# Kernel tuning notes

Hardware: AMD Instinct MI355X
Metric: run time of the kernel (lower is better)

## Reference

```python
import jax, jax.numpy as jnp
import numpy as np

D_EMBED = 768
N_HEAD = 12
D_ATTN = D_EMBED // N_HEAD  # 64
SCALE = 1.0 / np.sqrt(D_ATTN)


def setup_inputs() -> dict:
    key = jax.random.key(0)
    ks = jax.random.split(key, 5)
    B, S = 1, 4096
    x = jax.random.normal(ks[0], (B, S, D_EMBED), dtype=jnp.float32)
    # Linear weights stored as [in, out]; init std 0.02 as in _init_weights
    Wq = jax.random.normal(ks[1], (D_EMBED, D_EMBED), dtype=jnp.float32) * 0.02
    Wk = jax.random.normal(ks[2], (D_EMBED, D_EMBED), dtype=jnp.float32) * 0.02
    Wv = jax.random.normal(ks[3], (D_EMBED, D_EMBED), dtype=jnp.float32) * 0.02
    Wo = jax.random.normal(ks[4], (D_EMBED, D_EMBED), dtype=jnp.float32) * 0.02
    gamma = jnp.ones((N_HEAD,), dtype=jnp.float32)
    return {"x": x, "Wq": Wq, "Wk": Wk, "Wv": Wv, "Wo": Wo, "gamma": gamma}


def reference(x, Wq, Wk, Wv, Wo, gamma):
    B, S, _ = x.shape
    # QKV projections (self-attention: k = v = q = x)
    def split_heads(y):
        return y.reshape(B, S, N_HEAD, D_ATTN).transpose(0, 2, 1, 3)  # [B,H,S,D]
    q = split_heads(x @ Wq)
    k = split_heads(x @ Wk)
    v = split_heads(x @ Wv)
    # RBF attention scores: exp(-gamma * scale * ||q - k||^2)
    q_norm = jnp.sum(q * q, axis=-1, keepdims=True)            # [B,H,S,1]
    k_norm = jnp.sum(k * k, axis=-1, keepdims=True)            # [B,H,S,1]
    qk = jnp.einsum('bhsd,bhtd->bhst', q, k)                   # [B,H,S,S]
    dist = jnp.maximum(q_norm - 2.0 * qk + jnp.swapaxes(k_norm, -2, -1), 0.0)
    g = gamma.reshape(1, N_HEAD, 1, 1)
    scores = jnp.exp(-g * SCALE * dist)                        # [B,H,S,S]
    # attn @ V, merge heads, output proj (dropout p=0 -> identity)
    out = jnp.einsum('bhst,bhtd->bhsd', scores, v)
    out = out.transpose(0, 2, 1, 3).reshape(B, S, D_EMBED)
    return out @ Wo
```

## Files before the change

### kernel.cpp

```cpp
#include <hip/hip_runtime.h>
#include <stdint.h>


typedef __attribute__((ext_vector_type(4))) float f32x4;
typedef __attribute__((ext_vector_type(8))) short s16x8;
typedef __attribute__((ext_vector_type(2))) unsigned int u32x2;
typedef __attribute__((ext_vector_type(4))) unsigned int u32x4;

#define S_LEN 4096
#define NHEAD 12
#define DE 768

__device__ __forceinline__ uint16_t f2bf(float f) {
  unsigned u = __float_as_uint(f);
  u += 0x7fffu + ((u >> 16) & 1u);
  return (uint16_t)(u >> 16);
}

__device__ __forceinline__ unsigned cvt_pk_bf16(float a, float b) {
  unsigned r;
  asm("v_cvt_pk_bf16_f32 %0, %1, %2" : "=v"(r) : "v"(a), "v"(b));
  return r;
}

__device__ __forceinline__ void gll16(const void* g, void* l) {
  __builtin_amdgcn_global_load_lds(
      (const __attribute__((address_space(1))) unsigned int*)g,
      (__attribute__((address_space(3))) unsigned int*)l, 16, 0, 0);
}

__global__ void k_cvt_x(const float* __restrict__ x, uint16_t* __restrict__ xb) {
  int i = (blockIdx.x * 256 + threadIdx.x) * 4;
  float4 v = *(const float4*)(x + i);
  u32x2 o;
  o.x = (unsigned)f2bf(v.x) | ((unsigned)f2bf(v.y) << 16);
  o.y = (unsigned)f2bf(v.z) | ((unsigned)f2bf(v.w) << 16);
  *(u32x2*)(xb + i) = o;
}

__global__ void k_cvt_w(const float* __restrict__ W0, const float* __restrict__ W1,
                        const float* __restrict__ W2, const float* __restrict__ W3,
                        uint16_t* __restrict__ T0, uint16_t* __restrict__ T1,
                        uint16_t* __restrict__ T2, uint16_t* __restrict__ T3) {
  __shared__ float tile[64][65];
  int z = blockIdx.z;
  const float* W = z == 0 ? W0 : z == 1 ? W1 : z == 2 ? W2 : W3;
  uint16_t* T = z == 0 ? T0 : z == 1 ? T1 : z == 2 ? T2 : T3;
  int r0 = blockIdx.y * 64, c0 = blockIdx.x * 64;
  int t = threadIdx.x;
#pragma unroll
  for (int ii = 0; ii < 16; ++ii) {
    int idx = ii * 256 + t;
    int r = idx >> 6, c = idx & 63;
    tile[r][c] = W[(r0 + r) * DE + c0 + c];
  }
  __syncthreads();
#pragma unroll
  for (int ii = 0; ii < 16; ++ii) {
    int idx = ii * 256 + t;
    int r = idx >> 6, c = idx & 63;
    T[(size_t)(c0 + r) * DE + (r0 + c)] = f2bf(tile[c][r]);
  }
}

template <int MODE>
__global__ __launch_bounds__(256) void k_gemm(
    const uint16_t* __restrict__ A, const uint16_t* __restrict__ B0,
    const uint16_t* __restrict__ B1, const uint16_t* __restrict__ B2,
    uint16_t* __restrict__ Oq, uint16_t* __restrict__ Ok, uint16_t* __restrict__ Ov,
    float* __restrict__ OF) {
  __shared__ __align__(16) uint16_t As[128 * 64];
  __shared__ __align__(16) uint16_t Bs[128 * 64];
  const int K = DE;
  int z = (MODE == 0) ? blockIdx.z : 0;
  const uint16_t* Bt = (MODE == 0) ? (z == 0 ? B0 : z == 1 ? B1 : B2) : B0;
  int m0 = blockIdx.x * 128, n0 = blockIdx.y * 128;
  int tid = threadIdx.x, lane = tid & 63, wid = tid >> 6;
  int G = lane >> 4, c = lane & 15;
  int wr = (wid >> 1) * 64, wc = (wid & 1) * 64;
  f32x4 acc[4][4] = {};
  const char* AsB = (const char*)As;
  const char* BsB = (const char*)Bs;
  for (int kt = 0; kt < K / 64; ++kt) {
#pragma unroll
    for (int i = 0; i < 4; ++i) {
      int L = (i * 256 + tid) * 16;
      int row = L >> 7, ch = (L >> 4) & 7;
      int gch = ch ^ (row & 7);
      gll16((const char*)A + ((size_t)(m0 + row) * K + kt * 64) * 2 + gch * 16,
            (char*)As + i * 4096 + wid * 1024);
      gll16((const char*)Bt + ((size_t)(n0 + row) * K + kt * 64) * 2 + gch * 16,
            (char*)Bs + i * 4096 + wid * 1024);
    }
    __syncthreads();
#pragma unroll
    for (int ks = 0; ks < 2; ++ks) {
      s16x8 a[4], b[4];
#pragma unroll
      for (int mi = 0; mi < 4; ++mi) {
        int row = wr + mi * 16 + c;
        a[mi] = *(const s16x8*)(AsB + row * 128 + (((G + 4 * ks) ^ (row & 7)) << 4));
      }
#pragma unroll
      for (int ni = 0; ni < 4; ++ni) {
        int row = wc + ni * 16 + c;
        b[ni] = *(const s16x8*)(BsB + row * 128 + (((G + 4 * ks) ^ (row & 7)) << 4));
      }
#pragma unroll
      for (int mi = 0; mi < 4; ++mi)
#pragma unroll
        for (int ni = 0; ni < 4; ++ni)
          acc[mi][ni] = __builtin_amdgcn_mfma_f32_16x16x32_bf16(a[mi], b[ni], acc[mi][ni], 0, 0, 0);
    }
    __syncthreads();
  }
#pragma unroll
  for (int mi = 0; mi < 4; ++mi) {
#pragma unroll
    for (int ni = 0; ni < 4; ++ni) {
      int r = m0 + wr + mi * 16 + G * 4;
      int n = n0 + wc + ni * 16 + c;
      if (MODE == 0) {
        int h = n >> 6, d = n & 63;
        if (z < 2) {
          uint16_t* O = (z == 0) ? Oq : Ok;
#pragma unroll
          for (int rr = 0; rr < 4; ++rr)
            O[((size_t)h * S_LEN + (r + rr)) * 64 + d] = f2bf(acc[mi][ni][rr]);
        } else {
          u32x2 pk;
          pk.x = (unsigned)f2bf(acc[mi][ni][0]) | ((unsigned)f2bf(acc[mi][ni][1]) << 16);
          pk.y = (unsigned)f2bf(acc[mi][ni][2]) | ((unsigned)f2bf(acc[mi][ni][3]) << 16);
          *(u32x2*)(Ov + ((size_t)(h * 64 + d)) * S_LEN + r) = pk;
        }
      } else {
#pragma unroll
        for (int rr = 0; rr < 4; ++rr) OF[(size_t)(r + rr) * DE + n] = acc[mi][ni][rr];
      }
    }
  }
}

__global__ void k_norm(const uint16_t* __restrict__ q, const uint16_t* __restrict__ k,
                       const float* __restrict__ gamma,
                       float* __restrict__ cqn, float* __restrict__ ckn) {
  int row = blockIdx.x * 256 + threadIdx.x;
  const int total = NHEAD * S_LEN;
  const uint16_t* src = (row < total) ? q : k;
  float* dst = (row < total) ? cqn : ckn;
  int r = (row < total) ? row : row - total;
  float coef = -gamma[r >> 12] * 0.18033688011112043f;
  const u32x4* p = (const u32x4*)(src + (size_t)r * 64);
  float s = 0.f;
#pragma unroll
  for (int i = 0; i < 8; ++i) {
    u32x4 v = p[i];
#pragma unroll
    for (int j = 0; j < 4; ++j) {
      unsigned w = v[j];
      float a = __uint_as_float(w << 16);
      float b = __uint_as_float(w & 0xffff0000u);
      s += a * a + b * b;
    }
  }
  dst[r] = coef * s;
}

__global__ __launch_bounds__(256, 3) void k_attn(
    const uint16_t* __restrict__ q, const uint16_t* __restrict__ k,
    const uint16_t* __restrict__ vT, const float* __restrict__ cqn,
    const float* __restrict__ ckn, const float* __restrict__ gamma,
    uint16_t* __restrict__ att) {
  __shared__ __align__(16) uint16_t Ks[128 * 64];
  __shared__ __align__(16) uint16_t Vs[64 * 128];
  __shared__ __align__(16) uint16_t Ps[4][32 * 64];
  __shared__ __align__(16) float cks[128];
  int h = blockIdx.y;
  int tid = threadIdx.x, lane = tid & 63, wid = tid >> 6;
  int G = lane >> 4, c = lane & 15;
  int wq = wid & 1, wkv = wid >> 1;
  int qg0 = blockIdx.x * 64 + wq * 32 + c;

  s16x8 qf[2][2];
  const char* qb0 = (const char*)(q + ((size_t)h * S_LEN + qg0) * 64);
#pragma unroll
  for (int ks = 0; ks < 2; ++ks) {
    qf[0][ks] = *(const s16x8*)(qb0 + ks * 64 + G * 16);
    qf[1][ks] = *(const s16x8*)(qb0 + 2048 + ks * 64 + G * 16);
  }
  float ebq0 = __builtin_amdgcn_exp2f(cqn[h * S_LEN + qg0]);
  float ebq1 = __builtin_amdgcn_exp2f(cqn[h * S_LEN + qg0 + 16]);
  float m2c = gamma[h] * 0.36067376022224085f;

  f32x4 oacc[4][2] = {};
  char* PsB = (char*)Ps[wid];
  const char* KsB = (const char*)Ks;
  const char* VsB = (const char*)Vs;
  const char* kbase = (const char*)(k + (size_t)h * S_LEN * 64);
  const char* vbase = (const char*)(vT + (size_t)h * 64 * S_LEN);
  const float* cknh = ckn + h * S_LEN;
  int swzP = c & 7;

  for (int kt = 0; kt < S_LEN / 128; ++kt) {
#pragma unroll
    for (int i = 0; i < 4; ++i) {
      int L = (i * 256 + tid) * 16;
      int row = L >> 7, ch = (L >> 4) & 7;
      gll16(kbase + (size_t)(kt * 128 + row) * 128 + ((ch ^ (row & 7)) << 4),
            (char*)Ks + i * 4096 + wid * 1024);
    }
#pragma unroll
    for (int i = 0; i < 4; ++i) {
      int L = (i * 256 + tid) * 16;
      int d = L >> 8, ch = (L >> 4) & 15;
      gll16(vbase + (size_t)d * 8192 + kt * 256 + ((ch ^ (d & 15)) << 4),
            (char*)Vs + i * 4096 + wid * 1024);
    }
    if (tid < 32) gll16((const char*)(cknh + kt * 128) + tid * 16, (char*)cks);
    __syncthreads();

    f32x4 sacc[4][2] = {};
    __builtin_amdgcn_s_setprio(1);
#pragma unroll
    for (int ks = 0; ks < 2; ++ks) {
#pragma unroll
      for (int fb = 0; fb < 4; ++fb) {
        int row = wkv * 64 + fb * 16 + c;
        s16x8 a = *(const s16x8*)(KsB + row * 128 + (((G + 4 * ks) ^ (row & 7)) << 4));
        sacc[fb][0] = __builtin_amdgcn_mfma_f32_16x16x32_bf16(a, qf[0][ks], sacc[fb][0], 0, 0, 0);
        sacc[fb][1] = __builtin_amdgcn_mfma_f32_16x16x32_bf16(a, qf[1][ks], sacc[fb][1], 0, 0, 0);
      }
    }
    __builtin_amdgcn_s_setprio(0);

#pragma unroll
    for (int fb = 0; fb < 4; ++fb) {
      f32x4 ck = *(const f32x4*)&cks[wkv * 64 + fb * 16 + G * 4];
#pragma unroll
      for (int qb = 0; qb < 2; ++qb) {
        f32x4 sv = sacc[fb][qb];
        float p0 = __builtin_amdgcn_exp2f(ck[0] + m2c * sv[0]);
        float p1 = __builtin_amdgcn_exp2f(ck[1] + m2c * sv[1]);
        float p2 = __builtin_amdgcn_exp2f(ck[2] + m2c * sv[2]);
        float p3 = __builtin_amdgcn_exp2f(ck[3] + m2c * sv[3]);
        u32x2 pw;
        pw.x = cvt_pk_bf16(p0, p1);
        pw.y = cvt_pk_bf16(p2, p3);
        *(u32x2*)(PsB + (qb * 16 + c) * 128 + (((2 * fb + (G >> 1)) ^ swzP) << 4) + (G & 1) * 8) = pw;
      }
    }

    __builtin_amdgcn_s_setprio(1);
#pragma unroll
    for (int ks = 0; ks < 2; ++ks) {
      s16x8 b0 = *(const s16x8*)(PsB + c * 128 + (((G + 4 * ks) ^ swzP) << 4));
      s16x8 b1 = *(const s16x8*)(PsB + (16 + c) * 128 + (((G + 4 * ks) ^ swzP) << 4));
#pragma unroll
      for (int fd = 0; fd < 4; ++fd) {
        int d = fd * 16 + c;
        s16x8 va = *(const s16x8*)(VsB + d * 256 + (((wkv * 8 + G + 4 * ks) ^ (d & 15)) << 4));
        oacc[fd][0] = __builtin_amdgcn_mfma_f32_16x16x32_bf16(va, b0, oacc[fd][0], 0, 0, 0);
        oacc[fd][1] = __builtin_amdgcn_mfma_f32_16x16x32_bf16(va, b1, oacc[fd][1], 0, 0, 0);
      }
    }
    __builtin_amdgcn_s_setprio(0);
    __syncthreads();
  }

  if (wkv == 1) {
    float* dst = (float*)Ks + wq * 2048;
#pragma unroll
    for (int fd = 0; fd < 4; ++fd)
#pragma unroll
      for (int qb = 0; qb < 2; ++qb)
#pragma unroll
        for (int r = 0; r < 4; ++r)
          dst[(fd * 16 + G * 4 + r) * 32 + qb * 16 + c] = oacc[fd][qb][r];
  }
  __syncthreads();
  if (wkv == 0) {
    const float* srcp = (const float*)Ks + wq * 2048;
#pragma unroll
    for (int fd = 0; fd < 4; ++fd) {
#pragma unroll
      for (int qb = 0; qb < 2; ++qb) {
        float eb = qb ? ebq1 : ebq0;
        f32x4 v;
#pragma unroll
        for (int r = 0; r < 4; ++r)
          v[r] = (oacc[fd][qb][r] + srcp[(fd * 16 + G * 4 + r) * 32 + qb * 16 + c]) * eb;
        u32x2 w;
        w.x = cvt_pk_bf16(v[0], v[1]);
        w.y = cvt_pk_bf16(v[2], v[3]);
        *(u32x2*)(att + (size_t)(qg0 + qb * 16) * DE + h * 64 + fd * 16 + G * 4) = w;
      }
    }
  }
}

extern "C" void kernel_launch(void* const* d_in, const int* in_sizes, int n_in,
                              void* d_out, int out_size, void* d_ws, size_t ws_size,
                              hipStream_t stream) {
  (void)in_sizes; (void)n_in; (void)out_size; (void)ws_size;
  const float* x = (const float*)d_in[0];
  const float* Wq = (const float*)d_in[1];
  const float* Wk = (const float*)d_in[2];
  const float* Wv = (const float*)d_in[3];
  const float* Wo = (const float*)d_in[4];
  const float* gamma = (const float*)d_in[5];

  char* ws = (char*)d_ws;
  uint16_t* xb  = (uint16_t*)(ws);
  uint16_t* wqt = (uint16_t*)(ws + 6291456);
  uint16_t* wkt = (uint16_t*)(ws + 7471104);
  uint16_t* wvt = (uint16_t*)(ws + 8650752);
  uint16_t* wot = (uint16_t*)(ws + 9830400);
  uint16_t* qb  = (uint16_t*)(ws + 11010048);
  uint16_t* kb  = (uint16_t*)(ws + 17301504);
  uint16_t* vTb = (uint16_t*)(ws + 23592960);
  uint16_t* att = (uint16_t*)(ws + 29884416);
  float* cqn = (float*)(ws + 36175872);
  float* ckn = (float*)(ws + 36372480);

  k_cvt_x<<<3072, 256, 0, stream>>>(x, xb);
  k_cvt_w<<<dim3(12, 12, 4), 256, 0, stream>>>(Wq, Wk, Wv, Wo, wqt, wkt, wvt, wot);
  k_gemm<0><<<dim3(32, 6, 3), 256, 0, stream>>>(xb, wqt, wkt, wvt, qb, kb, vTb, nullptr);
  k_norm<<<384, 256, 0, stream>>>(qb, kb, gamma, cqn, ckn);
  k_attn<<<dim3(64, 12), 256, 0, stream>>>(qb, kb, vTb, cqn, ckn, gamma, att);
  k_gemm<1><<<dim3(32, 6, 1), 256, 0, stream>>>(att, wot, nullptr, nullptr,
                                                nullptr, nullptr, nullptr, (float*)d_out);
}
```

Baseline: 130.8 us.

## Register-prefetch next K/V tile while computing current tile

```diff
diff --git a/kernel.cpp b/kernel.cpp
--- a/kernel.cpp
+++ b/kernel.cpp
@@ -201,23 +201,41 @@
   const float* cknh = ckn + h * S_LEN;
   int swzP = c & 7;
 
+  u32x4 kr[4], vr[4];
+  f32x4 ckr;
+#pragma unroll
+  for (int i = 0; i < 4; ++i) {
+    int L = (i * 256 + tid) * 16;
+    int row = L >> 7, ch = (L >> 4) & 7;
+    kr[i] = *(const u32x4*)(kbase + (size_t)row * 128 + ((ch ^ (row & 7)) << 4));
+    int d = L >> 8, ch2 = (L >> 4) & 15;
+    vr[i] = *(const u32x4*)(vbase + (size_t)d * 8192 + ((ch2 ^ (d & 15)) << 4));
+  }
+  if (tid < 32) ckr = *(const f32x4*)(cknh + tid * 4);
+
   for (int kt = 0; kt < S_LEN / 128; ++kt) {
+    asm volatile("s_waitcnt lgkmcnt(0)" ::: "memory");
+    __builtin_amdgcn_s_barrier();
 #pragma unroll
     for (int i = 0; i < 4; ++i) {
-      int L = (i * 256 + tid) * 16;
-      int row = L >> 7, ch = (L >> 4) & 7;
-      gll16(kbase + (size_t)(kt * 128 + row) * 128 + ((ch ^ (row & 7)) << 4),
-            (char*)Ks + i * 4096 + wid * 1024);
-    }
-#pragma unroll
-    for (int i = 0; i < 4; ++i) {
-      int L = (i * 256 + tid) * 16;
-      int d = L >> 8, ch = (L >> 4) & 15;
-      gll16(vbase + (size_t)d * 8192 + kt * 256 + ((ch ^ (d & 15)) << 4),
-            (char*)Vs + i * 4096 + wid * 1024);
-    }
-    if (tid < 32) gll16((const char*)(cknh + kt * 128) + tid * 16, (char*)cks);
-    __syncthreads();
+      *(u32x4*)((char*)Ks + (i * 256 + tid) * 16) = kr[i];
+      *(u32x4*)((char*)Vs + (i * 256 + tid) * 16) = vr[i];
+    }
+    if (tid < 32) *(f32x4*)(cks + tid * 4) = ckr;
+    if (kt + 1 < S_LEN / 128) {
+#pragma unroll
+      for (int i = 0; i < 4; ++i) {
+        int L = (i * 256 + tid) * 16;
+        int row = L >> 7, ch = (L >> 4) & 7;
+        kr[i] = *(const u32x4*)(kbase + (size_t)(kt * 128 + 128 + row) * 128 + ((ch ^ (row & 7)) << 4));
+        int d = L >> 8, ch2 = (L >> 4) & 15;
+        vr[i] = *(const u32x4*)(vbase + (size_t)d * 8192 + kt * 256 + 256 + ((ch2 ^ (d & 15)) << 4));
+      }
+      if (tid < 32) ckr = *(const f32x4*)(cknh + kt * 128 + 128 + tid * 4);
+    }
+    asm volatile("s_waitcnt lgkmcnt(0)" ::: "memory");
+    __builtin_amdgcn_s_barrier();
+    __builtin_amdgcn_sched_barrier(0);
 
     f32x4 sacc[4][2] = {};
     __builtin_amdgcn_s_setprio(1);
@@ -264,9 +282,9 @@
       }
     }
     __builtin_amdgcn_s_setprio(0);
-    __syncthreads();
-  }
-
+  }
+
+  __syncthreads();
   if (wkv == 1) {
     float* dst = (float*)Ks + wq * 2048;
 #pragma unroll
```

Result: slower. 134.5 us (+2.8%).
